# Kernel optimization log

Measured on AMD Instinct MI355X. Metric: run time of the kernel, lower is better.

The kernel has to match this reference:

```python
import jax, jax.numpy as jnp
import numpy as np

TAU = 32.0
ALPHA = 0.9
B, C, F = 4096, 512, 128  # batch, n_classes, n_bits


def setup_inputs() -> dict:
    key = jax.random.key(0)
    k1, k2, k3, k4 = jax.random.split(key, 4)
    X = jax.random.normal(k1, (B, F), dtype=jnp.float32)
    T = jax.random.randint(k2, (B, C), 0, 2).astype(jnp.int32)  # 0/1 multi-label
    # kaiming_normal_(mode='fan_out') on a [C, F] tensor -> std = sqrt(2 / C)
    std = np.sqrt(2.0 / C).astype(np.float32)
    means = jax.random.normal(k3, (C, F), dtype=jnp.float32) * std
    log_vars = jax.random.normal(k4, (C, F), dtype=jnp.float32) * std
    return {"X": X, "T": T, "means": means, "log_vars": log_vars}


def _l2_normalize(x, eps=1e-12):
    # matches torch F.normalize(p=2): x / max(||x||, eps)
    n = jnp.sqrt(jnp.sum(x * x, axis=-1, keepdims=True))
    return x / jnp.maximum(n, eps)


def _mahalanobis(Xn, mu, log_vars):
    # M[i,j] = sum_f (x_if - mu_jf)^2 / exp(lv_jf)
    # expanded into three GEMM-like terms -> never materializes [N,C,F]
    inv = jnp.exp(-log_vars)                         # [C, F]
    t1 = (Xn * Xn) @ inv.T                           # [N, C]
    t2 = Xn @ (mu * inv).T                           # [N, C]
    t3 = jnp.sum(mu * mu * inv, axis=-1)             # [C]
    return t1 - 2.0 * t2 + t3[None, :]


def reference(X, T, means, log_vars):
    lv = jnp.clip(log_vars, 0.0, 6.0)                # relu6
    Xn = _l2_normalize(X)
    mu = _l2_normalize(means)
    D = _mahalanobis(Xn, mu, lv)                     # [N, C]

    P_all = jax.nn.softmax(-TAU * D, axis=1)         # [N, C]
    Tf = T.astype(X.dtype)
    P_sum = jnp.sum(P_all * Tf, axis=1)              # [N]
    nz = P_sum != 0
    safe = jnp.where(nz, P_sum, 1.0)
    loss = -jnp.sum(jnp.where(nz, jnp.log(safe), 0.0)) / jnp.maximum(
        jnp.sum(nz).astype(X.dtype), 1.0)

    # classes present in the batch (concrete mask -> static column selection)
    cw = np.asarray(jnp.sum(T, axis=0) != 0)
    Dc = D[:, cw]                                    # [N, Ccw]
    Tc = Tf[:, cw]
    S = Tc + jnp.exp(-ALPHA * Dc) * (1.0 - Tc)
    return (loss, S)
```

## Files before the change

kernel.cpp:

```cpp
#include <hip/hip_runtime.h>
#include <hip/hip_bf16.h>
#include <math.h>

#define NB 4096
#define NC 512
#define NF 128
#define NK 256
#define TAUc 32.0f
#define ALPHAc 0.9f

typedef __attribute__((ext_vector_type(8))) short bf16x8;
typedef __attribute__((ext_vector_type(4))) float f32x4;

__device__ inline void splitbf(float x, short& hi, short& lo) {
  unsigned u = __float_as_uint(x);
  hi = (short)(u >> 16);
  float l = x - __uint_as_float(u & 0xFFFF0000u);
  lo = (short)(__float_as_uint(l) >> 16);
}

__global__ __launch_bounds__(512) void k_zero(int* __restrict__ colnz) {
  colnz[threadIdx.x] = 0;
}

__global__ __launch_bounds__(256) void k_mask(const int* __restrict__ T,
                                              int* __restrict__ colnz) {
  int r0 = blockIdx.x * 16;
  int a0 = 0, a1 = 0;
  for (int r = 0; r < 16; ++r) {
    const int* row = T + (size_t)(r0 + r) * NC;
    a0 |= row[threadIdx.x];
    a1 |= row[threadIdx.x + 256];
  }
  if (a0) atomicOr(colnz + threadIdx.x, 1);
  if (a1) atomicOr(colnz + threadIdx.x + 256, 1);
}

__global__ __launch_bounds__(512) void k_scan(const int* __restrict__ colnz,
                                              int* __restrict__ pos) {
  __shared__ int s[NC];
  int t = threadIdx.x;
  int f = colnz[t] ? 1 : 0;
  s[t] = f;
  __syncthreads();
  for (int o = 1; o < NC; o <<= 1) {
    int add = (t >= o) ? s[t - o] : 0;
    __syncthreads();
    s[t] += add;
    __syncthreads();
  }
  pos[t] = s[t] - f;
}

__global__ __launch_bounds__(512) void k_fused(const float* __restrict__ X,
                                               const int* __restrict__ T,
                                               const float* __restrict__ means,
                                               const float* __restrict__ logv,
                                               const int* __restrict__ colnz,
                                               const int* __restrict__ pos,
                                               float* __restrict__ Sout,
                                               float* __restrict__ rowm,
                                               float* __restrict__ rowz,
                                               float* __restrict__ rowp,
                                               int Csel, int ident) {
  __shared__ __align__(16) unsigned char smB[131072];
  __shared__ float t3s[128];
  __shared__ float partm[2][64], partz[2][64], partp[2][64];
  int tid = threadIdx.x;
  int lane = tid & 63, w = tid >> 6;
  int wm = w & 3, wn = w >> 2;
  int lr = lane & 15, kq = lane >> 4;
  int bx = blockIdx.x;
  int gc = bx & 3, gr = bx >> 2;
  int r0 = gr * 64, c0 = gc * 128;

  int cls = w * 16 + (lane >> 2);
  int q = lane & 3;
  int c15 = (lane >> 2) & 15;
  float mua[32], lva[32];
  {
    const float4* mp = (const float4*)(means + (size_t)(c0 + cls) * NF + 32 * q);
    const float4* lp = (const float4*)(logv + (size_t)(c0 + cls) * NF + 32 * q);
    #pragma unroll
    for (int i = 0; i < 8; ++i) {
      *(float4*)(mua + 4 * i) = mp[i];
      *(float4*)(lva + 4 * i) = lp[i];
    }
  }

  float xv[4][8];
  {
    const float* xrow = X + (size_t)(r0 + wm * 16 + lr) * NF + 8 * kq;
    #pragma unroll
    for (int c = 0; c < 4; ++c) {
      float4 u0 = *(const float4*)(xrow + 32 * c);
      float4 u1 = *(const float4*)(xrow + 32 * c + 4);
      xv[c][0] = u0.x; xv[c][1] = u0.y; xv[c][2] = u0.z; xv[c][3] = u0.w;
      xv[c][4] = u1.x; xv[c][5] = u1.y; xv[c][6] = u1.z; xv[c][7] = u1.w;
    }
  }
  int tfv[4][4];
  #pragma unroll
  for (int i = 0; i < 4; ++i) {
    const int* tr = T + (size_t)(r0 + wm * 16 + 4 * kq + i) * NC + c0 + wn * 64 + lr;
    #pragma unroll
    for (int t = 0; t < 4; ++t) tfv[t][i] = tr[16 * t];
  }

  {
    float s = 0.f;
    #pragma unroll
    for (int k = 0; k < 32; ++k) s = fmaf(mua[k], mua[k], s);
    s += __shfl_xor(s, 1, 64);
    s += __shfl_xor(s, 2, 64);
    float rn_c = 1.0f / fmaxf(sqrtf(s), 1e-12f);
    float t3a = 0.f;
    #pragma unroll
    for (int i8 = 0; i8 < 4; ++i8) {
      bf16x8 h1, l1, h2, l2;
      #pragma unroll
      for (int j = 0; j < 8; ++j) {
        int jj = i8 * 8 + j;
        float ivv = __expf(-fminf(fmaxf(lva[jj], 0.f), 6.f));
        float m = mua[jj] * rn_c;
        short h, l;
        splitbf(ivv, h, l);
        h1[j] = h; l1[j] = l;
        splitbf(-2.f * m * ivv, h, l);
        h2[j] = h; l2[j] = l;
        t3a = fmaf(m * m, ivv, t3a);
      }
      unsigned e1 = (unsigned)((w * 8 + q) * 512 + i8 * 128 + c15 * 8) * 2u;
      unsigned e2 = (unsigned)((w * 8 + 4 + q) * 512 + i8 * 128 + c15 * 8) * 2u;
      *(bf16x8*)(smB + e1) = h1;
      *(bf16x8*)(smB + 65536 + e1) = l1;
      *(bf16x8*)(smB + e2) = h2;
      *(bf16x8*)(smB + 65536 + e2) = l2;
    }
    t3a += __shfl_xor(t3a, 1, 64);
    t3a += __shfl_xor(t3a, 2, 64);
    if (q == 0) t3s[cls] = t3a;
  }

  bf16x8 Afh[8], Afl[8];
  {
    float rsum = 0.f;
    #pragma unroll
    for (int c = 0; c < 4; ++c)
      #pragma unroll
      for (int j = 0; j < 8; ++j) rsum = fmaf(xv[c][j], xv[c][j], rsum);
    rsum += __shfl_xor(rsum, 16, 64);
    rsum += __shfl_xor(rsum, 32, 64);
    float rn = 1.0f / fmaxf(sqrtf(rsum), 1e-12f);
    #pragma unroll
    for (int c = 0; c < 4; ++c) {
      #pragma unroll
      for (int j = 0; j < 8; ++j) {
        float xn = xv[c][j] * rn;
        short h, l;
        splitbf(xn * xn, h, l);
        Afh[c][j] = h; Afl[c][j] = l;
        splitbf(xn, h, l);
        Afh[c + 4][j] = h; Afl[c + 4][j] = l;
      }
    }
  }

  __syncthreads();

  f32x4 acc[4] = {};
  #pragma unroll
  for (int k8 = 0; k8 < 8; ++k8) {
    #pragma unroll
    for (int t = 0; t < 4; ++t) {
      unsigned off = (unsigned)((((wn * 4 + t) * 8 + k8) * 64 + lane) * 16);
      bf16x8 bh = *(const bf16x8*)(smB + off);
      bf16x8 bl = *(const bf16x8*)(smB + 65536 + off);
      acc[t] = __builtin_amdgcn_mfma_f32_16x16x32_bf16(Afh[k8], bh, acc[t], 0, 0, 0);
      acc[t] = __builtin_amdgcn_mfma_f32_16x16x32_bf16(Afl[k8], bh, acc[t], 0, 0, 0);
      acc[t] = __builtin_amdgcn_mfma_f32_16x16x32_bf16(Afh[k8], bl, acc[t], 0, 0, 0);
    }
  }

  float d[4][4];
  #pragma unroll
  for (int t = 0; t < 4; ++t) {
    float tt = t3s[wn * 64 + 16 * t + lr];
    #pragma unroll
    for (int i = 0; i < 4; ++i) d[t][i] = acc[t][i] + tt;
  }

  float m4[4], Zi[4], Pi[4];
  #pragma unroll
  for (int i = 0; i < 4; ++i) {
    float mm = fminf(fminf(d[0][i], d[1][i]), fminf(d[2][i], d[3][i]));
    #pragma unroll
    for (int o = 1; o < 16; o <<= 1) mm = fminf(mm, __shfl_xor(mm, o, 64));
    float Z = 0.f, P = 0.f;
    #pragma unroll
    for (int t = 0; t < 4; ++t) {
      float p = __expf(TAUc * (mm - d[t][i]));
      Z += p;
      if (tfv[t][i]) P += p;
    }
    #pragma unroll
    for (int o = 1; o < 16; o <<= 1) { Z += __shfl_xor(Z, o, 64); P += __shfl_xor(P, o, 64); }
    m4[i] = mm; Zi[i] = Z; Pi[i] = P;
  }

  if (ident) {
    #pragma unroll
    for (int i = 0; i < 4; ++i) {
      float* srow = Sout + (size_t)(r0 + wm * 16 + 4 * kq + i) * NC + c0 + wn * 64 + lr;
      #pragma unroll
      for (int t = 0; t < 4; ++t)
        srow[16 * t] = tfv[t][i] ? 1.0f : __expf(-ALPHAc * d[t][i]);
    }
  } else {
    #pragma unroll
    for (int i = 0; i < 4; ++i) {
      float* srow = Sout + (size_t)(r0 + wm * 16 + 4 * kq + i) * Csel;
      #pragma unroll
      for (int t = 0; t < 4; ++t) {
        int c = c0 + wn * 64 + 16 * t + lr;
        if (colnz[c]) srow[pos[c]] = tfv[t][i] ? 1.0f : __expf(-ALPHAc * d[t][i]);
      }
    }
  }

  if (lr == 0) {
    #pragma unroll
    for (int i = 0; i < 4; ++i) {
      int row = wm * 16 + 4 * kq + i;
      partm[wn][row] = m4[i];
      partz[wn][row] = Zi[i];
      partp[wn][row] = Pi[i];
    }
  }
  __syncthreads();
  if (tid < 64) {
    float m0 = partm[0][tid], m1 = partm[1][tid];
    float m = fminf(m0, m1);
    float e0 = __expf(TAUc * (m - m0)), e1 = __expf(TAUc * (m - m1));
    int g = (r0 + tid) * 4 + gc;
    rowm[g] = m;
    rowz[g] = partz[0][tid] * e0 + partz[1][tid] * e1;
    rowp[g] = partp[0][tid] * e0 + partp[1][tid] * e1;
  }
}

__global__ __launch_bounds__(1024) void k_fin(const float* __restrict__ rowm,
                                              const float* __restrict__ rowz,
                                              const float* __restrict__ rowp,
                                              float* __restrict__ out) {
  __shared__ float sl[16];
  __shared__ int sc[16];
  int tid = threadIdx.x;
  int lane = tid & 63, w = tid >> 6;
  float ls = 0.f; int lc = 0;
  for (int r = tid; r < NB; r += 1024) {
    float4 mv = ((const float4*)rowm)[r];
    float4 zv = ((const float4*)rowz)[r];
    float4 pv = ((const float4*)rowp)[r];
    float m = fminf(fminf(mv.x, mv.y), fminf(mv.z, mv.w));
    float e0 = __expf(TAUc * (m - mv.x));
    float e1 = __expf(TAUc * (m - mv.y));
    float e2 = __expf(TAUc * (m - mv.z));
    float e3 = __expf(TAUc * (m - mv.w));
    float Z = zv.x * e0 + zv.y * e1 + zv.z * e2 + zv.w * e3;
    float P = pv.x * e0 + pv.y * e1 + pv.z * e2 + pv.w * e3;
    float Ps = P / Z;
    if (Ps > 0.f) { ls += logf(Ps); ++lc; }
  }
  #pragma unroll
  for (int o = 1; o < 64; o <<= 1) { ls += __shfl_xor(ls, o, 64); lc += __shfl_xor(lc, o, 64); }
  if (lane == 0) { sl[w] = ls; sc[w] = lc; }
  __syncthreads();
  if (tid == 0) {
    float s = 0.f; int c = 0;
    #pragma unroll
    for (int i = 0; i < 16; ++i) { s += sl[i]; c += sc[i]; }
    out[0] = -s / fmaxf((float)c, 1.0f);
  }
}

extern "C" void kernel_launch(void* const* d_in, const int* in_sizes, int n_in,
                              void* d_out, int out_size, void* d_ws, size_t ws_size,
                              hipStream_t stream) {
  const float* X     = (const float*)d_in[0];
  const int*   T     = (const int*)d_in[1];
  const float* means = (const float*)d_in[2];
  const float* logv  = (const float*)d_in[3];
  float* out = (float*)d_out;
  char* ws = (char*)d_ws;

  float*  rowm = (float*) (ws);
  float*  rowz = (float*) (ws + 65536);
  float*  rowp = (float*) (ws + 131072);
  int*    colnz= (int*)   (ws + 196608);
  int*    pos  = (int*)   (ws + 198656);

  int Csel = (out_size - 1) / NB;
  int ident = (Csel == NC);

  if (!ident) {
    k_zero<<<1, NC, 0, stream>>>(colnz);
    k_mask<<<NB / 16, 256, 0, stream>>>(T, colnz);
    k_scan<<<1, NC, 0, stream>>>(colnz, pos);
  }
  k_fused<<<256, 512, 0, stream>>>(X, T, means, logv, colnz, pos,
                                   out + 1, rowm, rowz, rowp, Csel, ident);
  k_fin<<<1, 1024, 0, stream>>>(rowm, rowz, rowp, out);
}
```

Before: 22.12 us.

## Split fused kernel into 64x64 tiles with 256-thread blocks

Each fused block now handles 64 rows by 64 classes instead of 128 classes, giving 512 blocks of 256 threads. This halves LDS use per block (64KB) and doubles grid size for better CU coverage on a 256-CU part. In-block cross-wave softmax merging is removed, so each block writes 8 partials per row and the finalize kernel merges 8 instead of 4. The cost is recomputing X normalization and the A fragments twice as often, plus double the partial-statistics traffic.

```diff
diff --git a/kernel.cpp b/kernel.cpp
--- a/kernel.cpp
+++ b/kernel.cpp
@@ -52,7 +52,7 @@
   pos[t] = s[t] - f;
 }
 
-__global__ __launch_bounds__(512) void k_fused(const float* __restrict__ X,
+__global__ __launch_bounds__(256) void k_fused(const float* __restrict__ X,
                                                const int* __restrict__ T,
                                                const float* __restrict__ means,
                                                const float* __restrict__ logv,
@@ -63,20 +63,18 @@
                                                float* __restrict__ rowz,
                                                float* __restrict__ rowp,
                                                int Csel, int ident) {
-  __shared__ __align__(16) unsigned char smB[131072];
-  __shared__ float t3s[128];
-  __shared__ float partm[2][64], partz[2][64], partp[2][64];
+  __shared__ __align__(16) unsigned char smB[65536];
+  __shared__ float t3s[64];
   int tid = threadIdx.x;
   int lane = tid & 63, w = tid >> 6;
-  int wm = w & 3, wn = w >> 2;
   int lr = lane & 15, kq = lane >> 4;
   int bx = blockIdx.x;
-  int gc = bx & 3, gr = bx >> 2;
-  int r0 = gr * 64, c0 = gc * 128;
+  int gc = bx & 7, gr = bx >> 3;
+  int r0 = gr * 64, c0 = gc * 64;
 
   int cls = w * 16 + (lane >> 2);
   int q = lane & 3;
-  int c15 = (lane >> 2) & 15;
+  int lr2 = lane >> 2;
   float mua[32], lva[32];
   {
     const float4* mp = (const float4*)(means + (size_t)(c0 + cls) * NF + 32 * q);
@@ -90,7 +88,7 @@
 
   float xv[4][8];
   {
-    const float* xrow = X + (size_t)(r0 + wm * 16 + lr) * NF + 8 * kq;
+    const float* xrow = X + (size_t)(r0 + w * 16 + lr) * NF + 8 * kq;
     #pragma unroll
     for (int c = 0; c < 4; ++c) {
       float4 u0 = *(const float4*)(xrow + 32 * c);
@@ -102,7 +100,7 @@
   int tfv[4][4];
   #pragma unroll
   for (int i = 0; i < 4; ++i) {
-    const int* tr = T + (size_t)(r0 + wm * 16 + 4 * kq + i) * NC + c0 + wn * 64 + lr;
+    const int* tr = T + (size_t)(r0 + w * 16 + 4 * kq + i) * NC + c0 + lr;
     #pragma unroll
     for (int t = 0; t < 4; ++t) tfv[t][i] = tr[16 * t];
   }
@@ -116,11 +114,11 @@
     float rn_c = 1.0f / fmaxf(sqrtf(s), 1e-12f);
     float t3a = 0.f;
     #pragma unroll
-    for (int i8 = 0; i8 < 4; ++i8) {
+    for (int kq2 = 0; kq2 < 4; ++kq2) {
       bf16x8 h1, l1, h2, l2;
       #pragma unroll
       for (int j = 0; j < 8; ++j) {
-        int jj = i8 * 8 + j;
+        int jj = kq2 * 8 + j;
         float ivv = __expf(-fminf(fmaxf(lva[jj], 0.f), 6.f));
         float m = mua[jj] * rn_c;
         short h, l;
@@ -130,12 +128,12 @@
         h2[j] = h; l2[j] = l;
         t3a = fmaf(m * m, ivv, t3a);
       }
-      unsigned e1 = (unsigned)((w * 8 + q) * 512 + i8 * 128 + c15 * 8) * 2u;
-      unsigned e2 = (unsigned)((w * 8 + 4 + q) * 512 + i8 * 128 + c15 * 8) * 2u;
+      unsigned e1 = (unsigned)(((w * 8 + q) * 64 + kq2 * 16 + lr2) * 16);
+      unsigned e2 = (unsigned)(((w * 8 + 4 + q) * 64 + kq2 * 16 + lr2) * 16);
       *(bf16x8*)(smB + e1) = h1;
-      *(bf16x8*)(smB + 65536 + e1) = l1;
+      *(bf16x8*)(smB + 32768 + e1) = l1;
       *(bf16x8*)(smB + e2) = h2;
-      *(bf16x8*)(smB + 65536 + e2) = l2;
+      *(bf16x8*)(smB + 32768 + e2) = l2;
     }
     t3a += __shfl_xor(t3a, 1, 64);
     t3a += __shfl_xor(t3a, 2, 64);
@@ -173,9 +171,9 @@
   for (int k8 = 0; k8 < 8; ++k8) {
     #pragma unroll
     for (int t = 0; t < 4; ++t) {
-      unsigned off = (unsigned)((((wn * 4 + t) * 8 + k8) * 64 + lane) * 16);
+      unsigned off = (unsigned)(((t * 8 + k8) * 64 + lane) * 16);
       bf16x8 bh = *(const bf16x8*)(smB + off);
-      bf16x8 bl = *(const bf16x8*)(smB + 65536 + off);
+      bf16x8 bl = *(const bf16x8*)(smB + 32768 + off);
       acc[t] = __builtin_amdgcn_mfma_f32_16x16x32_bf16(Afh[k8], bh, acc[t], 0, 0, 0);
       acc[t] = __builtin_amdgcn_mfma_f32_16x16x32_bf16(Afl[k8], bh, acc[t], 0, 0, 0);
       acc[t] = __builtin_amdgcn_mfma_f32_16x16x32_bf16(Afh[k8], bl, acc[t], 0, 0, 0);
@@ -185,7 +183,7 @@
   float d[4][4];
   #pragma unroll
   for (int t = 0; t < 4; ++t) {
-    float tt = t3s[wn * 64 + 16 * t + lr];
+    float tt = t3s[16 * t + lr];
     #pragma unroll
     for (int i = 0; i < 4; ++i) d[t][i] = acc[t][i] + tt;
   }
@@ -211,7 +209,7 @@
   if (ident) {
     #pragma unroll
     for (int i = 0; i < 4; ++i) {
-      float* srow = Sout + (size_t)(r0 + wm * 16 + 4 * kq + i) * NC + c0 + wn * 64 + lr;
+      float* srow = Sout + (size_t)(r0 + w * 16 + 4 * kq + i) * NC + c0 + lr;
       #pragma unroll
       for (int t = 0; t < 4; ++t)
         srow[16 * t] = tfv[t][i] ? 1.0f : __expf(-ALPHAc * d[t][i]);
@@ -219,10 +217,10 @@
   } else {
     #pragma unroll
     for (int i = 0; i < 4; ++i) {
-      float* srow = Sout + (size_t)(r0 + wm * 16 + 4 * kq + i) * Csel;
+      float* srow = Sout + (size_t)(r0 + w * 16 + 4 * kq + i) * Csel;
       #pragma unroll
       for (int t = 0; t < 4; ++t) {
-        int c = c0 + wn * 64 + 16 * t + lr;
+        int c = c0 + 16 * t + lr;
         if (colnz[c]) srow[pos[c]] = tfv[t][i] ? 1.0f : __expf(-ALPHAc * d[t][i]);
       }
     }
@@ -231,21 +229,11 @@
   if (lr == 0) {
     #pragma unroll
     for (int i = 0; i < 4; ++i) {
-      int row = wm * 16 + 4 * kq + i;
-      partm[wn][row] = m4[i];
-      partz[wn][row] = Zi[i];
-      partp[wn][row] = Pi[i];
-    }
-  }
-  __syncthreads();
-  if (tid < 64) {
-    float m0 = partm[0][tid], m1 = partm[1][tid];
-    float m = fminf(m0, m1);
-    float e0 = __expf(TAUc * (m - m0)), e1 = __expf(TAUc * (m - m1));
-    int g = (r0 + tid) * 4 + gc;
-    rowm[g] = m;
-    rowz[g] = partz[0][tid] * e0 + partz[1][tid] * e1;
-    rowp[g] = partp[0][tid] * e0 + partp[1][tid] * e1;
+      int g = (r0 + w * 16 + 4 * kq + i) * 8 + gc;
+      rowm[g] = m4[i];
+      rowz[g] = Zi[i];
+      rowp[g] = Pi[i];
+    }
   }
 }
 
@@ -259,16 +247,26 @@
   int lane = tid & 63, w = tid >> 6;
   float ls = 0.f; int lc = 0;
   for (int r = tid; r < NB; r += 1024) {
-    float4 mv = ((const float4*)rowm)[r];
-    float4 zv = ((const float4*)rowz)[r];
-    float4 pv = ((const float4*)rowp)[r];
-    float m = fminf(fminf(mv.x, mv.y), fminf(mv.z, mv.w));
-    float e0 = __expf(TAUc * (m - mv.x));
-    float e1 = __expf(TAUc * (m - mv.y));
-    float e2 = __expf(TAUc * (m - mv.z));
-    float e3 = __expf(TAUc * (m - mv.w));
-    float Z = zv.x * e0 + zv.y * e1 + zv.z * e2 + zv.w * e3;
-    float P = pv.x * e0 + pv.y * e1 + pv.z * e2 + pv.w * e3;
+    float4 m0 = ((const float4*)rowm)[2 * r];
+    float4 m1 = ((const float4*)rowm)[2 * r + 1];
+    float4 z0 = ((const float4*)rowz)[2 * r];
+    float4 z1 = ((const float4*)rowz)[2 * r + 1];
+    float4 p0 = ((const float4*)rowp)[2 * r];
+    float4 p1 = ((const float4*)rowp)[2 * r + 1];
+    float m = fminf(fminf(fminf(m0.x, m0.y), fminf(m0.z, m0.w)),
+                    fminf(fminf(m1.x, m1.y), fminf(m1.z, m1.w)));
+    float Z = 0.f, P = 0.f;
+    {
+      float e;
+      e = __expf(TAUc * (m - m0.x)); Z += z0.x * e; P += p0.x * e;
+      e = __expf(TAUc * (m - m0.y)); Z += z0.y * e; P += p0.y * e;
+      e = __expf(TAUc * (m - m0.z)); Z += z0.z * e; P += p0.z * e;
+      e = __expf(TAUc * (m - m0.w)); Z += z0.w * e; P += p0.w * e;
+      e = __expf(TAUc * (m - m1.x)); Z += z1.x * e; P += p1.x * e;
+      e = __expf(TAUc * (m - m1.y)); Z += z1.y * e; P += p1.y * e;
+      e = __expf(TAUc * (m - m1.z)); Z += z1.z * e; P += p1.z * e;
+      e = __expf(TAUc * (m - m1.w)); Z += z1.w * e; P += p1.w * e;
+    }
     float Ps = P / Z;
     if (Ps > 0.f) { ls += logf(Ps); ++lc; }
   }
@@ -295,10 +293,10 @@
   char* ws = (char*)d_ws;
 
   float*  rowm = (float*) (ws);
-  float*  rowz = (float*) (ws + 65536);
-  float*  rowp = (float*) (ws + 131072);
-  int*    colnz= (int*)   (ws + 196608);
-  int*    pos  = (int*)   (ws + 198656);
+  float*  rowz = (float*) (ws + 131072);
+  float*  rowp = (float*) (ws + 262144);
+  int*    colnz= (int*)   (ws + 393216);
+  int*    pos  = (int*)   (ws + 395264);
 
   int Csel = (out_size - 1) / NB;
   int ident = (Csel == NC);
@@ -308,7 +306,7 @@
     k_mask<<<NB / 16, 256, 0, stream>>>(T, colnz);
     k_scan<<<1, NC, 0, stream>>>(colnz, pos);
   }
-  k_fused<<<256, 512, 0, stream>>>(X, T, means, logv, colnz, pos,
+  k_fused<<<512, 256, 0, stream>>>(X, T, means, logv, colnz, pos,
                                    out + 1, rowm, rowz, rowp, Csel, ident);
   k_fin<<<1, 1024, 0, stream>>>(rowm, rowz, rowp, out);
 }
```

Result: slower. 25.12 us (+13.5%).
